# Performance work log

Measured on AMD Instinct MI355X. Metric: run time of the kernel, lower is better.

Reference implementation:

```python
import jax, jax.numpy as jnp
import numpy as np

N_NODES = 50000


def _sage_conv(x, src, dst, W_l, b_l, W_r):
    # PyG SAGEConv (aggr='mean'): out = lin_l(mean_{j in N(i)} x_j) + lin_r(x_i)
    # lin_l has bias, lin_r has no bias.
    neigh_sum = jax.ops.segment_sum(x[src], dst, num_segments=N_NODES)  # [N, F]
    deg = jax.ops.segment_sum(jnp.ones_like(dst, dtype=x.dtype), dst, num_segments=N_NODES)
    neigh_mean = neigh_sum / jnp.maximum(deg, 1.0)[:, None]
    return neigh_mean @ W_l.T + b_l + x @ W_r.T


def setup_inputs() -> dict:
    key = jax.random.key(0)
    ks = jax.random.split(key, 8)
    D, H, C = 768, 128, 4
    x = jax.random.normal(ks[0], (N_NODES, D), dtype=jnp.float32)
    edge_index = jax.random.randint(ks[1], (2, 800000), 0, N_NODES, dtype=jnp.int64)
    s1 = 1.0 / np.sqrt(D)
    s2 = 1.0 / np.sqrt(H)
    return {
        "x": x,
        "edge_index": edge_index,
        "W1_l": jax.random.uniform(ks[2], (H, D), jnp.float32, -s1, s1),
        "b1_l": jnp.zeros((H,), jnp.float32),
        "W1_r": jax.random.uniform(ks[3], (H, D), jnp.float32, -s1, s1),
        "W2_l": jax.random.uniform(ks[4], (C, H), jnp.float32, -s2, s2),
        "b2_l": jnp.zeros((C,), jnp.float32),
        "W2_r": jax.random.uniform(ks[5], (C, H), jnp.float32, -s2, s2),
    }


def reference(x, edge_index, W1_l, b1_l, W1_r, W2_l, b2_l, W2_r):
    src, dst = edge_index[0], edge_index[1]
    h = jax.nn.relu(_sage_conv(x, src, dst, W1_l, b1_l, W1_r))  # [N, H]
    out = _sage_conv(h, src, dst, W2_l, b2_l, W2_r)  # [N, C]
    return out
```

## Files before the change

kernel.cpp:

```cpp
#include <hip/hip_runtime.h>


typedef __bf16 bf16x8 __attribute__((ext_vector_type(8)));
typedef float  f32x4  __attribute__((ext_vector_type(4)));

__device__ __forceinline__ float bf16_lo(uint32_t w) {
    union { uint32_t u; float f; } c; c.u = w << 16; return c.f;
}
__device__ __forceinline__ float bf16_hi(uint32_t w) {
    union { uint32_t u; float f; } c; c.u = w & 0xffff0000u; return c.f;
}

__device__ __forceinline__ void load_lds16(const void* g, void* l) {
    __builtin_amdgcn_global_load_lds(
        (const __attribute__((address_space(1))) void*)g,
        (__attribute__((address_space(3))) void*)l, 16, 0, 0);
}

__global__ __launch_bounds__(256)
void prep(const float* __restrict__ W1l, const float* __restrict__ W1r,
          __bf16* __restrict__ Bp, int* __restrict__ deg, int N)
{
    int i = blockIdx.x * 256 + threadIdx.x;
    if (i < N) deg[i] = 0;
    if (i < 256 * 768) {
        int col = i / 768, k = i - col * 768;
        float v = (col < 128) ? W1l[col * 768 + k] : W1r[(col - 128) * 768 + k];
        Bp[((k >> 3) << 11) + (col << 3) + (k & 7)] = (__bf16)v;
    }
}

__global__ __launch_bounds__(256)
void csr_count(const int* __restrict__ ei, int* __restrict__ deg, int E)
{
    int e = blockIdx.x * 256 + threadIdx.x;
    if (e >= E) return;
    atomicAdd(&deg[ei[E + e]], 1);
}

__global__ __launch_bounds__(1024)
void scan1(const int* __restrict__ deg, int* __restrict__ row_ptr,
           int* __restrict__ partials, int N)
{
    __shared__ int buf[1024];
    int i = blockIdx.x * 1024 + threadIdx.x;
    int v = (i < N) ? deg[i] : 0;
    int val = v;
    buf[threadIdx.x] = val;
    __syncthreads();
    for (int off = 1; off < 1024; off <<= 1) {
        int t = (threadIdx.x >= (unsigned)off) ? buf[threadIdx.x - off] : 0;
        __syncthreads();
        val += t;
        buf[threadIdx.x] = val;
        __syncthreads();
    }
    if (i < N) row_ptr[i] = val - v;
    if (threadIdx.x == 1023) partials[blockIdx.x] = val;
}

__global__ __launch_bounds__(1024)
void scan23(int* __restrict__ row_ptr, int* __restrict__ cursor,
            const int* __restrict__ partials, int N, int E, int nb)
{
    __shared__ int soff;
    int b = blockIdx.x;
    if (threadIdx.x < 64) {
        int lane = threadIdx.x;
        int v = (lane < nb) ? partials[lane] : 0;
        int s = v;
        #pragma unroll
        for (int off = 1; off < 64; off <<= 1) {
            int t = __shfl_up(s, off);
            if (lane >= off) s += t;
        }
        if (lane == b) soff = s - v;
    }
    __syncthreads();
    int off = soff;
    int i = b * 1024 + threadIdx.x;
    if (i < N) {
        int v = row_ptr[i] + off;
        row_ptr[i] = v;
        cursor[i]  = v;
    }
    if (b == 0 && threadIdx.x == 0) row_ptr[N] = E;
}

__global__ __launch_bounds__(512)
void gemm_fill(const float* __restrict__ x, const __bf16* __restrict__ Bp,
               __bf16* __restrict__ Cb, int M, int mtiles,
               const int* __restrict__ ei, int* __restrict__ cursor,
               int* __restrict__ csr_src, int E)
{
    __shared__ float As[3][64][64];
    const int tid = threadIdx.x;

    if ((int)blockIdx.x >= mtiles) {
        int stride = (gridDim.x - mtiles) * 512;
        for (int e = (blockIdx.x - mtiles) * 512 + tid; e < E; e += stride) {
            int src = ei[e];
            int dst = ei[E + e];
            int pos = atomicAdd(&cursor[dst], 1);
            csr_src[pos] = src;
        }
        return;
    }

    const int bm   = blockIdx.x * 64;
    const int lane = tid & 63;
    const int wave = tid >> 6;
    const int wr = wave >> 2, wc = wave & 3;
    const int l15 = lane & 15;
    const int lk  = lane >> 4;

    f32x4 acc[2][4] = {};

    const int sr0 = wave * 8 + (lane >> 4);
    const int sr1 = wave * 8 + 4 + (lane >> 4);
    const int sc  = lane & 15;
    const float* g0 = x + (size_t)min(bm + sr0, M - 1) * 768 + ((sc ^ (sr0 & 7)) << 2);
    const float* g1 = x + (size_t)min(bm + sr1, M - 1) * 768 + ((sc ^ (sr1 & 7)) << 2);

    const __bf16* bbase = Bp + ((size_t)(wc * 64 + l15) << 3) + ((size_t)lk << 11);

    load_lds16(g0,      &As[0][wave * 8][0]);
    load_lds16(g1,      &As[0][wave * 8 + 4][0]);
    load_lds16(g0 + 64, &As[1][wave * 8][0]);
    load_lds16(g1 + 64, &As[1][wave * 8 + 4][0]);

    for (int kt = 0; kt < 12; ++kt) {
        asm volatile("s_waitcnt vmcnt(2)\n\ts_barrier" ::: "memory");
        __builtin_amdgcn_sched_barrier(0);
        const int buf = kt % 3;

        bf16x8 bcur[2][4];
        #pragma unroll
        for (int ks = 0; ks < 2; ++ks)
            #pragma unroll
            for (int j = 0; j < 4; ++j)
                bcur[ks][j] = *(const bf16x8*)(bbase +
                    (((size_t)(kt * 8 + ks * 4) << 11) + ((size_t)j << 7)));

        if (kt < 10) {
            const int nb = (kt + 2) % 3;
            load_lds16(g0 + (kt + 2) * 64, &As[nb][wave * 8][0]);
            load_lds16(g1 + (kt + 2) * 64, &As[nb][wave * 8 + 4][0]);
        }

        #pragma unroll
        for (int ks = 0; ks < 2; ++ks) {
            bf16x8 af[2];
            #pragma unroll
            for (int i = 0; i < 2; ++i) {
                int r = wr * 32 + i * 16 + l15;
                int sw = r & 7;
                int c0 = (ks * 32 + lk * 8) >> 2;
                float4 lo = *(const float4*)&As[buf][r][((c0)     ^ sw) << 2];
                float4 hi = *(const float4*)&As[buf][r][((c0 + 1) ^ sw) << 2];
                bf16x8 a;
                a[0] = (__bf16)lo.x; a[1] = (__bf16)lo.y;
                a[2] = (__bf16)lo.z; a[3] = (__bf16)lo.w;
                a[4] = (__bf16)hi.x; a[5] = (__bf16)hi.y;
                a[6] = (__bf16)hi.z; a[7] = (__bf16)hi.w;
                af[i] = a;
            }
            #pragma unroll
            for (int i = 0; i < 2; ++i)
                #pragma unroll
                for (int j = 0; j < 4; ++j)
                    acc[i][j] = __builtin_amdgcn_mfma_f32_16x16x32_bf16(
                        af[i], bcur[ks][j], acc[i][j], 0, 0, 0);
        }
    }

    #pragma unroll
    for (int i = 0; i < 2; ++i)
        #pragma unroll
        for (int j = 0; j < 4; ++j)
            #pragma unroll
            for (int v = 0; v < 4; ++v) {
                int row = bm + wr * 32 + i * 16 + lk * 4 + v;
                int col = wc * 64 + j * 16 + l15;
                if (row < M) Cb[(size_t)row * 256 + col] = (__bf16)acc[i][j][v];
            }
}

__global__ __launch_bounds__(256)
void sage1_fused(const int* __restrict__ row_ptr, const int* __restrict__ csr_src,
                 const __bf16* __restrict__ pq, const float* __restrict__ b1,
                 const float* __restrict__ W2l, const float* __restrict__ W2r,
                 float* __restrict__ r, float* __restrict__ s, int N)
{
    __shared__ float Wl[512], Wr[512];
    for (int i = threadIdx.x; i < 512; i += 256) {
        Wl[i] = W2l[i];
        Wr[i] = W2r[i];
    }
    __syncthreads();

    int wid  = threadIdx.x >> 6;
    int lane = threadIdx.x & 63;
    int g = lane >> 3;
    int l = lane & 7;
    int n = blockIdx.x * 4 + wid;
    if (n >= N) return;
    int beg = row_ptr[n], end = row_ptr[n + 1];

    float a0[8] = {}, a1[8] = {};
    for (int eb = beg; eb < end; eb += 64) {
        int cnt = min(64, end - eb);
        int id = (eb + lane < end) ? csr_src[eb + lane] : 0;
        for (int t = 0; t < cnt; t += 8) {
            int src = __shfl(id, t + g);
            if (t + g < cnt) {
                const __bf16* row = pq + (size_t)src * 256;
                uint4 w0 = *(const uint4*)(row + l * 8);
                uint4 w1 = *(const uint4*)(row + 64 + l * 8);
                a0[0] += bf16_lo(w0.x); a0[1] += bf16_hi(w0.x);
                a0[2] += bf16_lo(w0.y); a0[3] += bf16_hi(w0.y);
                a0[4] += bf16_lo(w0.z); a0[5] += bf16_hi(w0.z);
                a0[6] += bf16_lo(w0.w); a0[7] += bf16_hi(w0.w);
                a1[0] += bf16_lo(w1.x); a1[1] += bf16_hi(w1.x);
                a1[2] += bf16_lo(w1.y); a1[3] += bf16_hi(w1.y);
                a1[4] += bf16_lo(w1.z); a1[5] += bf16_hi(w1.z);
                a1[6] += bf16_lo(w1.w); a1[7] += bf16_hi(w1.w);
            }
        }
    }
    #pragma unroll
    for (int c = 0; c < 8; ++c) {
        a0[c] += __shfl_xor(a0[c], 8);  a1[c] += __shfl_xor(a1[c], 8);
        a0[c] += __shfl_xor(a0[c], 16); a1[c] += __shfl_xor(a1[c], 16);
        a0[c] += __shfl_xor(a0[c], 32); a1[c] += __shfl_xor(a1[c], 32);
    }

    float inv = 1.0f / fmaxf((float)(end - beg), 1.0f);
    const __bf16* qrow = pq + (size_t)n * 256 + 128;
    uint4  qw0 = *(const uint4*)(qrow + l * 8);
    uint4  qw1 = *(const uint4*)(qrow + 64 + l * 8);
    float4 bv00 = *(const float4*)(b1 + l * 8);
    float4 bv01 = *(const float4*)(b1 + l * 8 + 4);
    float4 bv10 = *(const float4*)(b1 + 64 + l * 8);
    float4 bv11 = *(const float4*)(b1 + 64 + l * 8 + 4);
    float h0[8], h1[8];
    h0[0] = fmaxf(a0[0] * inv + bv00.x + bf16_lo(qw0.x), 0.f);
    h0[1] = fmaxf(a0[1] * inv + bv00.y + bf16_hi(qw0.x), 0.f);
    h0[2] = fmaxf(a0[2] * inv + bv00.z + bf16_lo(qw0.y), 0.f);
    h0[3] = fmaxf(a0[3] * inv + bv00.w + bf16_hi(qw0.y), 0.f);
    h0[4] = fmaxf(a0[4] * inv + bv01.x + bf16_lo(qw0.z), 0.f);
    h0[5] = fmaxf(a0[5] * inv + bv01.y + bf16_hi(qw0.z), 0.f);
    h0[6] = fmaxf(a0[6] * inv + bv01.z + bf16_lo(qw0.w), 0.f);
    h0[7] = fmaxf(a0[7] * inv + bv01.w + bf16_hi(qw0.w), 0.f);
    h1[0] = fmaxf(a1[0] * inv + bv10.x + bf16_lo(qw1.x), 0.f);
    h1[1] = fmaxf(a1[1] * inv + bv10.y + bf16_hi(qw1.x), 0.f);
    h1[2] = fmaxf(a1[2] * inv + bv10.z + bf16_lo(qw1.y), 0.f);
    h1[3] = fmaxf(a1[3] * inv + bv10.w + bf16_hi(qw1.y), 0.f);
    h1[4] = fmaxf(a1[4] * inv + bv11.x + bf16_lo(qw1.z), 0.f);
    h1[5] = fmaxf(a1[5] * inv + bv11.y + bf16_hi(qw1.z), 0.f);
    h1[6] = fmaxf(a1[6] * inv + bv11.z + bf16_lo(qw1.w), 0.f);
    h1[7] = fmaxf(a1[7] * inv + bv11.w + bf16_hi(qw1.w), 0.f);

    float part[8];
    #pragma unroll
    for (int c = 0; c < 4; ++c) {
        float pl = 0.f, pr = 0.f;
        #pragma unroll
        for (int j = 0; j < 8; ++j) {
            pl = fmaf(h0[j], Wl[c * 128 + l * 8 + j], pl);
            pl = fmaf(h1[j], Wl[c * 128 + 64 + l * 8 + j], pl);
            pr = fmaf(h0[j], Wr[c * 128 + l * 8 + j], pr);
            pr = fmaf(h1[j], Wr[c * 128 + 64 + l * 8 + j], pr);
        }
        part[c] = pl; part[4 + c] = pr;
    }
    #pragma unroll
    for (int off = 4; off; off >>= 1)
        #pragma unroll
        for (int c = 0; c < 8; ++c)
            part[c] += __shfl_xor(part[c], off);
    if (lane == 0) {
        *(float4*)(r + (size_t)n * 4) = make_float4(part[0], part[1], part[2], part[3]);
        *(float4*)(s + (size_t)n * 4) = make_float4(part[4], part[5], part[6], part[7]);
    }
}

__global__ __launch_bounds__(256)
void sage2_gather(const int* __restrict__ row_ptr, const int* __restrict__ csr_src,
                  const float* __restrict__ r, const float* __restrict__ s,
                  const float* __restrict__ b2, float* __restrict__ out, int N)
{
    int t = blockIdx.x * 256 + threadIdx.x;
    if (t >= N * 4) return;
    int n = t >> 2, c = t & 3;
    int beg = row_ptr[n], end = row_ptr[n + 1];
    float acc = 0.f;
    for (int e = beg; e < end; ++e)
        acc += r[(size_t)csr_src[e] * 4 + c];
    out[t] = acc / fmaxf((float)(end - beg), 1.0f) + b2[c] + s[t];
}

extern "C" void kernel_launch(void* const* d_in, const int* in_sizes, int n_in,
                              void* d_out, int out_size, void* d_ws, size_t ws_size,
                              hipStream_t stream)
{
    const float* x   = (const float*)d_in[0];
    const int*   ei  = (const int*)d_in[1];
    const float* W1l = (const float*)d_in[2];
    const float* b1l = (const float*)d_in[3];
    const float* W1r = (const float*)d_in[4];
    const float* W2l = (const float*)d_in[5];
    const float* b2l = (const float*)d_in[6];
    const float* W2r = (const float*)d_in[7];
    float* out = (float*)d_out;

    const int N = in_sizes[0] / 768;
    const int E = in_sizes[1] / 2;
    const int NB = (N + 1023) / 1024;
    const int mtiles = (N + 63) / 64;

    char* ws = (char*)d_ws;
    size_t off = 0;
    auto alloc = [&](size_t bytes) -> void* {
        void* pp = ws + off;
        off += (bytes + 255) & ~(size_t)255;
        return pp;
    };
    __bf16* pq      = (__bf16*)alloc((size_t)N * 256 * 2);
    float*  r       = (float*)alloc((size_t)N * 4 * 4);
    float*  s       = (float*)alloc((size_t)N * 4 * 4);
    __bf16* Bp      = (__bf16*)alloc((size_t)256 * 768 * 2);
    int*    deg     = (int*)alloc((size_t)N * 4);
    int*    row_ptr = (int*)alloc((size_t)(N + 1) * 4);
    int*    cursor  = (int*)alloc((size_t)N * 4);
    int*    csr_src = (int*)alloc((size_t)E * 4);
    int*    partials= (int*)alloc((size_t)64 * 4);

    prep<<<(256 * 768 + 255) / 256, 256, 0, stream>>>(W1l, W1r, Bp, deg, N);

    csr_count<<<(E + 255) / 256, 256, 0, stream>>>(ei, deg, E);
    scan1<<<NB, 1024, 0, stream>>>(deg, row_ptr, partials, N);
    scan23<<<NB, 1024, 0, stream>>>(row_ptr, cursor, partials, N, E, NB);

    gemm_fill<<<mtiles + 256, 512, 0, stream>>>(x, Bp, pq, N, mtiles,
                                                ei, cursor, csr_src, E);

    sage1_fused<<<(N + 3) / 4, 256, 0, stream>>>(row_ptr, csr_src, pq, b1l,
                                                 W2l, W2r, r, s, N);

    sage2_gather<<<(N * 4 + 255) / 256, 256, 0, stream>>>(row_ptr, csr_src, r, s, b2l, out, N);
}
```

Baseline: 203.8 us.

## Shrink GEMM tile to 32 rows, stage A as bf16 via registers

The GEMM part of gemm_fill goes from 64-row tiles with 512 threads and a triple-buffered fp32 LDS stage loaded by global_load_lds to 32-row tiles with 256 threads. A is now prefetched into registers, converted to bf16 once, and stored to a padded double-buffered bf16 LDS tile. This removes the repeated per-wave fp32-to-bf16 conversion of A fragments, cuts LDS use, and doubles the block count for occupancy. In exchange every B fragment is loaded from global memory by twice as many blocks, and the async LDS loads are replaced by synchronous register staging with a __syncthreads per k-step.

```diff
diff --git a/kernel.cpp b/kernel.cpp
--- a/kernel.cpp
+++ b/kernel.cpp
@@ -9,12 +9,6 @@
 }
 __device__ __forceinline__ float bf16_hi(uint32_t w) {
     union { uint32_t u; float f; } c; c.u = w & 0xffff0000u; return c.f;
-}
-
-__device__ __forceinline__ void load_lds16(const void* g, void* l) {
-    __builtin_amdgcn_global_load_lds(
-        (const __attribute__((address_space(1))) void*)g,
-        (__attribute__((address_space(3))) void*)l, 16, 0, 0);
 }
 
 __global__ __launch_bounds__(256)
@@ -87,18 +81,18 @@
     if (b == 0 && threadIdx.x == 0) row_ptr[N] = E;
 }
 
-__global__ __launch_bounds__(512)
+__global__ __launch_bounds__(256)
 void gemm_fill(const float* __restrict__ x, const __bf16* __restrict__ Bp,
                __bf16* __restrict__ Cb, int M, int mtiles,
                const int* __restrict__ ei, int* __restrict__ cursor,
                int* __restrict__ csr_src, int E)
 {
-    __shared__ float As[3][64][64];
+    __shared__ __bf16 As[2][32][72];
     const int tid = threadIdx.x;
 
     if ((int)blockIdx.x >= mtiles) {
-        int stride = (gridDim.x - mtiles) * 512;
-        for (int e = (blockIdx.x - mtiles) * 512 + tid; e < E; e += stride) {
+        int stride = (gridDim.x - mtiles) * 256;
+        for (int e = (blockIdx.x - mtiles) * 256 + tid; e < E; e += stride) {
             int src = ei[e];
             int dst = ei[E + e];
             int pos = atomicAdd(&cursor[dst], 1);
@@ -107,70 +101,57 @@
         return;
     }
 
-    const int bm   = blockIdx.x * 64;
+    const int bm   = blockIdx.x * 32;
     const int lane = tid & 63;
-    const int wave = tid >> 6;
-    const int wr = wave >> 2, wc = wave & 3;
-    const int l15 = lane & 15;
-    const int lk  = lane >> 4;
+    const int wc   = tid >> 6;
+    const int l15  = lane & 15;
+    const int lk   = lane >> 4;
 
     f32x4 acc[2][4] = {};
 
-    const int sr0 = wave * 8 + (lane >> 4);
-    const int sr1 = wave * 8 + 4 + (lane >> 4);
-    const int sc  = lane & 15;
-    const float* g0 = x + (size_t)min(bm + sr0, M - 1) * 768 + ((sc ^ (sr0 & 7)) << 2);
-    const float* g1 = x + (size_t)min(bm + sr1, M - 1) * 768 + ((sc ^ (sr1 & 7)) << 2);
+    const int srow = tid >> 3;
+    const int scol = (tid & 7) << 3;
+    const float* gsrc = x + (size_t)min(bm + srow, M - 1) * 768 + scol;
 
     const __bf16* bbase = Bp + ((size_t)(wc * 64 + l15) << 3) + ((size_t)lk << 11);
 
-    load_lds16(g0,      &As[0][wave * 8][0]);
-    load_lds16(g1,      &As[0][wave * 8 + 4][0]);
-    load_lds16(g0 + 64, &As[1][wave * 8][0]);
-    load_lds16(g1 + 64, &As[1][wave * 8 + 4][0]);
-
+    float4 ap0, ap1;
+    auto load_A = [&](int k0) {
+        ap0 = *(const float4*)(gsrc + k0);
+        ap1 = *(const float4*)(gsrc + k0 + 4);
+    };
+
+    load_A(0);
     for (int kt = 0; kt < 12; ++kt) {
-        asm volatile("s_waitcnt vmcnt(2)\n\ts_barrier" ::: "memory");
-        __builtin_amdgcn_sched_barrier(0);
-        const int buf = kt % 3;
-
-        bf16x8 bcur[2][4];
-        #pragma unroll
-        for (int ks = 0; ks < 2; ++ks)
+        const int buf = kt & 1;
+        {
+            bf16x8 b;
+            b[0] = (__bf16)ap0.x; b[1] = (__bf16)ap0.y;
+            b[2] = (__bf16)ap0.z; b[3] = (__bf16)ap0.w;
+            b[4] = (__bf16)ap1.x; b[5] = (__bf16)ap1.y;
+            b[6] = (__bf16)ap1.z; b[7] = (__bf16)ap1.w;
+            *(bf16x8*)&As[buf][srow][scol] = b;
+        }
+        __syncthreads();
+        if (kt < 11) load_A((kt + 1) * 64);
+
+        #pragma unroll
+        for (int ks = 0; ks < 2; ++ks) {
+            bf16x8 bcur[4];
             #pragma unroll
             for (int j = 0; j < 4; ++j)
-                bcur[ks][j] = *(const bf16x8*)(bbase +
+                bcur[j] = *(const bf16x8*)(bbase +
                     (((size_t)(kt * 8 + ks * 4) << 11) + ((size_t)j << 7)));
-
-        if (kt < 10) {
-            const int nb = (kt + 2) % 3;
-            load_lds16(g0 + (kt + 2) * 64, &As[nb][wave * 8][0]);
-            load_lds16(g1 + (kt + 2) * 64, &As[nb][wave * 8 + 4][0]);
-        }
-
-        #pragma unroll
-        for (int ks = 0; ks < 2; ++ks) {
             bf16x8 af[2];
             #pragma unroll
-            for (int i = 0; i < 2; ++i) {
-                int r = wr * 32 + i * 16 + l15;
-                int sw = r & 7;
-                int c0 = (ks * 32 + lk * 8) >> 2;
-                float4 lo = *(const float4*)&As[buf][r][((c0)     ^ sw) << 2];
-                float4 hi = *(const float4*)&As[buf][r][((c0 + 1) ^ sw) << 2];
-                bf16x8 a;
-                a[0] = (__bf16)lo.x; a[1] = (__bf16)lo.y;
-                a[2] = (__bf16)lo.z; a[3] = (__bf16)lo.w;
-                a[4] = (__bf16)hi.x; a[5] = (__bf16)hi.y;
-                a[6] = (__bf16)hi.z; a[7] = (__bf16)hi.w;
-                af[i] = a;
-            }
+            for (int i = 0; i < 2; ++i)
+                af[i] = *(const bf16x8*)&As[buf][i * 16 + l15][ks * 32 + lk * 8];
             #pragma unroll
             for (int i = 0; i < 2; ++i)
                 #pragma unroll
                 for (int j = 0; j < 4; ++j)
                     acc[i][j] = __builtin_amdgcn_mfma_f32_16x16x32_bf16(
-                        af[i], bcur[ks][j], acc[i][j], 0, 0, 0);
+                        af[i], bcur[j], acc[i][j], 0, 0, 0);
         }
     }
 
@@ -180,7 +161,7 @@
         for (int j = 0; j < 4; ++j)
             #pragma unroll
             for (int v = 0; v < 4; ++v) {
-                int row = bm + wr * 32 + i * 16 + lk * 4 + v;
+                int row = bm + i * 16 + lk * 4 + v;
                 int col = wc * 64 + j * 16 + l15;
                 if (row < M) Cb[(size_t)row * 256 + col] = (__bf16)acc[i][j][v];
             }
@@ -317,7 +298,7 @@
     const int N = in_sizes[0] / 768;
     const int E = in_sizes[1] / 2;
     const int NB = (N + 1023) / 1024;
-    const int mtiles = (N + 63) / 64;
+    const int mtiles = (N + 31) / 32;
 
     char* ws = (char*)d_ws;
     size_t off = 0;
@@ -342,7 +323,7 @@
     scan1<<<NB, 1024, 0, stream>>>(deg, row_ptr, partials, N);
     scan23<<<NB, 1024, 0, stream>>>(row_ptr, cursor, partials, N, E, NB);
 
-    gemm_fill<<<mtiles + 256, 512, 0, stream>>>(x, Bp, pq, N, mtiles,
+    gemm_fill<<<mtiles + 256, 256, 0, stream>>>(x, Bp, pq, N, mtiles,
                                                 ei, cursor, csr_src, E);
 
     sage1_fused<<<(N + 3) / 4, 256, 0, stream>>>(row_ptr, csr_src, pq, b1l,
```

Measured after the change: 202.9 us. Within noise of the previous version (-0.4%).
